# Performance work log

Hardware: AMD Instinct MI355X
Metric: run time of the kernel (lower is better)

## Reference

```python
import jax, jax.numpy as jnp
import numpy as np

N = 4096
IN_F = 256
F = 64      # out_features
H = 4       # heads
NEG_SLOPE = 0.2


def setup_inputs() -> dict:
    key = jax.random.key(0)
    k1, k2, k3, k4 = jax.random.split(key, 4)
    x = jax.random.normal(k1, (N, IN_F), dtype=jnp.float32)
    # symmetric random binary adjacency with self-loops (avoids empty softmax rows)
    adj = jax.random.bernoulli(k2, 0.5, (N, N)).astype(jnp.float32)
    adj = jnp.clip(adj + adj.T, 0.0, 1.0)
    adj = jnp.maximum(adj, jnp.eye(N, dtype=jnp.float32))
    W = jax.random.normal(k3, (IN_F, F * H), dtype=jnp.float32) * (1.0 / np.sqrt(IN_F))
    a = jax.random.normal(k4, (2 * F, 1), dtype=jnp.float32) * 0.1
    return {"x": x, "adj": adj, "W": W, "a": a}


def reference(x, adj, W, a):
    # h: [N, H, F]
    h = (x @ W).reshape(N, H, F)
    # e[i, j, h] = leakyrelu(a_l . h[i, h] + a_r . h[j, h])  -- avoids the O(N^2*H*2F) concat
    a_l = a[:F, 0]
    a_r = a[F:, 0]
    el = jnp.einsum('nhf,f->nh', h, a_l)  # [N, H]
    er = jnp.einsum('nhf,f->nh', h, a_r)  # [N, H]
    e = jax.nn.leaky_relu(el[:, None, :] + er[None, :, :], NEG_SLOPE)  # [N, N, H]
    e = jnp.where(adj[:, :, None] == 0, -jnp.inf, e)
    attention = jax.nn.softmax(e, axis=1)  # softmax over neighbors j
    h_prime = jnp.einsum('ijh,jhf->ihf', attention, h)  # [N, H, F]
    return h_prime.mean(axis=1)  # [N, F]  (heads > 1 -> mean over heads)
```

## Files before the change

kernel.cpp:

```cpp
#include <hip/hip_runtime.h>
#include <hip/hip_bf16.h>

#define NN 4096
#define LOG2E 1.44269504088896340736f
#define SPLITS 16

typedef __attribute__((ext_vector_type(8))) short s8v;
typedef __attribute__((ext_vector_type(4))) float f4v;

__device__ __forceinline__ unsigned fu(float x){ union{float f;unsigned u;}z; z.f=x; return z.u; }
__device__ __forceinline__ unsigned short f2bf_rne(float x){
  unsigned u = fu(x);
  u += 0x7fffu + ((u >> 16) & 1u);
  return (unsigned short)(u >> 16);
}
__device__ __forceinline__ unsigned pack2_rne(float a, float b){
  return (unsigned)f2bf_rne(a) | ((unsigned)f2bf_rne(b) << 16);
}

__global__ __launch_bounds__(256) void k1_proj(
    const float* __restrict__ x, const float* __restrict__ W,
    const float* __restrict__ a, unsigned short* __restrict__ Vf,
    float* __restrict__ el4, float* __restrict__ Qr, float* __restrict__ Sr)
{
  __shared__ float4 xs[512];
  const int t = threadIdx.x;
  const int r0 = blockIdx.x * 8;
  const float4* xg = (const float4*)(x + (size_t)r0 * 256);
  xs[t] = xg[t];
  xs[t + 256] = xg[t + 256];
  __syncthreads();

  float acc[8] = {0.f,0.f,0.f,0.f,0.f,0.f,0.f,0.f};
  const float* Wp = W + t;
  float w0 = Wp[0], w1 = Wp[256], w2 = Wp[512], w3 = Wp[768];
  #pragma unroll 1
  for (int k4 = 0; k4 < 64; ++k4) {
    const int kn = (k4 + 1) & 63;
    float nw0 = Wp[kn*1024 +   0];
    float nw1 = Wp[kn*1024 + 256];
    float nw2 = Wp[kn*1024 + 512];
    float nw3 = Wp[kn*1024 + 768];
    #pragma unroll
    for (int r = 0; r < 8; ++r) {
      float4 xv = xs[r*64 + k4];
      acc[r] = fmaf(xv.x, w0, acc[r]);
      acc[r] = fmaf(xv.y, w1, acc[r]);
      acc[r] = fmaf(xv.z, w2, acc[r]);
      acc[r] = fmaf(xv.w, w3, acc[r]);
    }
    w0 = nw0; w1 = nw1; w2 = nw2; w3 = nw3;
  }

  union { unsigned u[4]; s8v v; } pk;
  #pragma unroll
  for (int p = 0; p < 4; ++p)
    pk.u[p] = pack2_rne(acc[2*p], acc[2*p+1]);
  {
    const int hh = t >> 6, nf = (t >> 4) & 3, mm = t & 15;
    const int jblk = r0 >> 5, qq = (r0 >> 3) & 3;
    const size_t chunk = (size_t)(((hh * 128 + jblk) * 4 + nf) * 64 + qq * 16 + mm);
    *(s8v*)(Vf + chunk * 8) = pk.v;
  }

  const int f = t & 63, h = t >> 6;
  const float al = a[f], ar = a[64 + f];
  #pragma unroll
  for (int r = 0; r < 8; ++r) {
    float v = acc[r] * al;
    float u = acc[r] * ar;
    #pragma unroll
    for (int off = 32; off > 0; off >>= 1) {
      v += __shfl_xor(v, off);
      u += __shfl_xor(u, off);
    }
    if (f == 0) {
      el4[(r0 + r) * 4 + h] = v * LOG2E;
      float up = u * LOG2E;
      Qr[h * NN + (r0 + r)] = __builtin_amdgcn_exp2f(up);
      Sr[h * NN + (r0 + r)] = __builtin_amdgcn_exp2f(0.2f * up);
    }
  }
}

__global__ __launch_bounds__(256, 4) void k0_pack(
    const float* __restrict__ adj, const float* __restrict__ el4,
    const float* __restrict__ Qr, const float* __restrict__ Sr,
    unsigned long long* __restrict__ adjB,
    float* __restrict__ PL, float* __restrict__ RL)
{
  const int t = threadIdx.x;
  const int w = t >> 6, l = t & 63;
  const int row = blockIdx.x * 4 + w;
  const float* arow = adj + (size_t)row * NN;

  float4 elv = *(const float4*)(el4 + row * 4);
  const float P[4] = { __builtin_amdgcn_exp2f(elv.x), __builtin_amdgcn_exp2f(elv.y),
                       __builtin_amdgcn_exp2f(elv.z), __builtin_amdgcn_exp2f(elv.w) };
  const float R[4] = { __builtin_amdgcn_exp2f(0.2f*elv.x), __builtin_amdgcn_exp2f(0.2f*elv.y),
                       __builtin_amdgcn_exp2f(0.2f*elv.z), __builtin_amdgcn_exp2f(0.2f*elv.w) };
  float lsum[4] = {0.f, 0.f, 0.f, 0.f};

  float4 av, qv0, qv1, qv2, qv3, sv0, sv1, sv2, sv3;
  av  = *(const float4*)(arow + l * 4);
  qv0 = *(const float4*)(Qr + 0 * NN + l * 4);
  qv1 = *(const float4*)(Qr + 1 * NN + l * 4);
  qv2 = *(const float4*)(Qr + 2 * NN + l * 4);
  qv3 = *(const float4*)(Qr + 3 * NN + l * 4);
  sv0 = *(const float4*)(Sr + 0 * NN + l * 4);
  sv1 = *(const float4*)(Sr + 1 * NN + l * 4);
  sv2 = *(const float4*)(Sr + 2 * NN + l * 4);
  sv3 = *(const float4*)(Sr + 3 * NN + l * 4);

  #pragma unroll 1
  for (int p = 0; p < 16; ++p) {
    const int nb = ((p < 15) ? (p + 1) * 256 : 0) + l * 4;
    float4 nav  = *(const float4*)(arow + nb);
    float4 nqv0 = *(const float4*)(Qr + 0 * NN + nb);
    float4 nqv1 = *(const float4*)(Qr + 1 * NN + nb);
    float4 nqv2 = *(const float4*)(Qr + 2 * NN + nb);
    float4 nqv3 = *(const float4*)(Qr + 3 * NN + nb);
    float4 nsv0 = *(const float4*)(Sr + 0 * NN + nb);
    float4 nsv1 = *(const float4*)(Sr + 1 * NN + nb);
    float4 nsv2 = *(const float4*)(Sr + 2 * NN + nb);
    float4 nsv3 = *(const float4*)(Sr + 3 * NN + nb);

    unsigned long long b0 = __ballot(av.x != 0.0f);
    unsigned long long b1 = __ballot(av.y != 0.0f);
    unsigned long long b2 = __ballot(av.z != 0.0f);
    unsigned long long b3 = __ballot(av.w != 0.0f);
    if (l == 0) {
      unsigned long long* dst = adjB + (size_t)row * 64 + p * 4;
      dst[0] = b0; dst[1] = b1; dst[2] = b2; dst[3] = b3;
    }
    #pragma unroll
    for (int h = 0; h < 4; ++h) {
      const float4 qv = (h==0)?qv0:(h==1)?qv1:(h==2)?qv2:qv3;
      const float4 sv = (h==0)?sv0:(h==1)?sv1:(h==2)?sv2:sv3;
      float m0 = fmaxf(P[h] * qv.x, R[h] * sv.x);
      float m1 = fmaxf(P[h] * qv.y, R[h] * sv.y);
      float m2 = fmaxf(P[h] * qv.z, R[h] * sv.z);
      float m3 = fmaxf(P[h] * qv.w, R[h] * sv.w);
      lsum[h] = fmaf(av.x, m0, lsum[h]);
      lsum[h] = fmaf(av.y, m1, lsum[h]);
      lsum[h] = fmaf(av.z, m2, lsum[h]);
      lsum[h] = fmaf(av.w, m3, lsum[h]);
    }
    av = nav;
    qv0 = nqv0; qv1 = nqv1; qv2 = nqv2; qv3 = nqv3;
    sv0 = nsv0; sv1 = nsv1; sv2 = nsv2; sv3 = nsv3;
  }

  #pragma unroll
  for (int h = 0; h < 4; ++h) {
    float v = lsum[h];
    #pragma unroll
    for (int off = 32; off > 0; off >>= 1) v += __shfl_xor(v, off);
    lsum[h] = v;
  }
  if (l < 4) {
    float li = 1.0f / lsum[l];
    PL[row * 4 + l] = P[l] * li;
    RL[row * 4 + l] = R[l] * li;
  }
}

__global__ __launch_bounds__(256, 4) void k2_attn(
    const unsigned long long* __restrict__ adjB, const unsigned short* __restrict__ Vf,
    const float* __restrict__ PL, const float* __restrict__ RL,
    const float* __restrict__ Qr, const float* __restrict__ Sr,
    float* __restrict__ out)
{
  __shared__ float qs[2048];
  const int t = threadIdx.x;
  const int w = t >> 6, l = t & 63;
  const int m = l & 15, q = l >> 4;
  const int i0 = blockIdx.x * 64;
  const int split = blockIdx.y;
  const int i = i0 + w * 16 + m;
  const int jwin = split * 256;

  {
    const int h = t >> 6;
    float4 qv = *(const float4*)(Qr + h * NN + jwin + l * 4);
    float4 sv = *(const float4*)(Sr + h * NN + jwin + l * 4);
    const int jc = l >> 3, qq = (l >> 1) & 3, hp = (l & 1) * 4;
    float* cell = qs + ((h * 8 + jc) * 4 + qq) * 16;
    *(float4*)(cell + hp) = qv;
    *(float4*)(cell + 8 + hp) = sv;
  }

  float4 pl4 = *(const float4*)(PL + i * 4);
  float4 rl4 = *(const float4*)(RL + i * 4);
  const float Pl[4] = {pl4.x, pl4.y, pl4.z, pl4.w};
  const float Rl[4] = {rl4.x, rl4.y, rl4.z, rl4.w};

  const unsigned long long* bp = adjB + (size_t)i * 64 + split * 4;
  unsigned long long b0 = bp[0], b1 = bp[1], b2 = bp[2], b3 = bp[3];

  f4v acc[4];
  #pragma unroll
  for (int nf = 0; nf < 4; ++nf) acc[nf] = (f4v){0.f, 0.f, 0.f, 0.f};

  const s8v* vfp = (const s8v*)Vf;
  s8v Bc[4];
  #pragma unroll
  for (int nf = 0; nf < 4; ++nf)
    Bc[nf] = vfp[(size_t)((0 * 128 + split * 8 + 0) * 4 + nf) * 64 + l];

  __syncthreads();

  #pragma unroll 1
  for (int jc = 0; jc < 8; ++jc) {
    const unsigned sh = jc * 8 + q * 2;
    const unsigned t0 = (unsigned)(b0 >> sh) & 3u;
    const unsigned t1 = (unsigned)(b1 >> sh) & 3u;
    const unsigned t2 = (unsigned)(b2 >> sh) & 3u;
    const unsigned t3 = (unsigned)(b3 >> sh) & 3u;
    float bitf[8];
    bitf[0] = (float)(t0 & 1u); bitf[4] = (float)(t0 >> 1);
    bitf[1] = (float)(t1 & 1u); bitf[5] = (float)(t1 >> 1);
    bitf[2] = (float)(t2 & 1u); bitf[6] = (float)(t2 >> 1);
    bitf[3] = (float)(t3 & 1u); bitf[7] = (float)(t3 >> 1);

    #pragma unroll
    for (int h = 0; h < 4; ++h) {
      const int hn = (h < 3) ? h + 1 : 0;
      const int jcn = (h < 3) ? jc : jc + 1;
      s8v Bn[4];
      #pragma unroll
      for (int nf = 0; nf < 4; ++nf)
        Bn[nf] = vfp[(size_t)((hn * 128 + split * 8 + jcn) * 4 + nf) * 64 + l];

      const float* cell = qs + ((h * 8 + jc) * 4 + q) * 16;
      float4 q0  = *(const float4*)(cell);
      float4 q1  = *(const float4*)(cell + 4);
      float4 sv0 = *(const float4*)(cell + 8);
      float4 sv1 = *(const float4*)(cell + 12);
      const float Ph = Pl[h], Rh = Rl[h];
      float s0 = bitf[0] * fmaxf(Ph * q0.x, Rh * sv0.x);
      float s1 = bitf[1] * fmaxf(Ph * q0.y, Rh * sv0.y);
      float s2 = bitf[2] * fmaxf(Ph * q0.z, Rh * sv0.z);
      float s3 = bitf[3] * fmaxf(Ph * q0.w, Rh * sv0.w);
      float s4 = bitf[4] * fmaxf(Ph * q1.x, Rh * sv1.x);
      float s5 = bitf[5] * fmaxf(Ph * q1.y, Rh * sv1.y);
      float s6 = bitf[6] * fmaxf(Ph * q1.z, Rh * sv1.z);
      float s7 = bitf[7] * fmaxf(Ph * q1.w, Rh * sv1.w);
      union { unsigned u[4]; s8v v; } A;
      A.u[0] = pack2_rne(s0, s1);
      A.u[1] = pack2_rne(s2, s3);
      A.u[2] = pack2_rne(s4, s5);
      A.u[3] = pack2_rne(s6, s7);
      #pragma unroll
      for (int nf = 0; nf < 4; ++nf)
        acc[nf] = __builtin_amdgcn_mfma_f32_16x16x32_bf16(A.v, Bc[nf], acc[nf], 0, 0, 0);
      #pragma unroll
      for (int nf = 0; nf < 4; ++nf) Bc[nf] = Bn[nf];
    }
  }

  #pragma unroll
  for (int nf = 0; nf < 4; ++nf)
    #pragma unroll
    for (int r = 0; r < 4; ++r) {
      int row = i0 + w * 16 + q * 4 + r;
      int col = nf * 16 + m;
      atomicAdd(&out[row * 64 + col], 0.25f * acc[nf][r]);
    }
}

extern "C" void kernel_launch(void* const* d_in, const int* in_sizes, int n_in,
                              void* d_out, int out_size, void* d_ws, size_t ws_size,
                              hipStream_t stream) {
  const float* x   = (const float*)d_in[0];
  const float* adj = (const float*)d_in[1];
  const float* W   = (const float*)d_in[2];
  const float* a   = (const float*)d_in[3];
  float* out = (float*)d_out;

  char* ws = (char*)d_ws;
  unsigned short* Vf = (unsigned short*)ws;
  float* el4 = (float*)(ws + (2u << 20));
  float* Qr  = (float*)(ws + (2u << 20) + (64u << 10));
  float* Sr  = (float*)(ws + (2u << 20) + (128u << 10));
  float* PLp = (float*)(ws + (2u << 20) + (192u << 10));
  float* RLp = (float*)(ws + (2u << 20) + (256u << 10));
  unsigned long long* adjB = (unsigned long long*)(ws + (2u << 20) + (320u << 10));

  hipMemsetAsync(out, 0, (size_t)out_size * sizeof(float), stream);
  k1_proj<<<512, 256, 0, stream>>>(x, W, a, Vf, el4, Qr, Sr);
  k0_pack<<<1024, 256, 0, stream>>>(adj, el4, Qr, Sr, adjB, PLp, RLp);
  k2_attn<<<dim3(64, SPLITS), 256, 0, stream>>>(adjB, Vf, PLp, RLp, Qr, Sr, out);
}
```

Before: 175.4 us.

## Remap attention waves to split the neighbor axis and reduce partials in LDS

In the attention kernel, the four waves of a block now take 16 rows each over four different 256-column neighbor windows, where before they took four row groups over one shared window. Each wave stages its own Q/S window in a larger shared buffer, which removes the early barrier. Partial accumulators are summed across waves in LDS before one wave issues the atomics, so global atomic traffic drops by a factor of four. The cost is four times the LDS footprint, which may lower occupancy, and less reuse of the Vf tiles across waves in a block.

```diff
diff --git a/kernel.cpp b/kernel.cpp
--- a/kernel.cpp
+++ b/kernel.cpp
@@ -3,7 +3,6 @@
 
 #define NN 4096
 #define LOG2E 1.44269504088896340736f
-#define SPLITS 16
 
 typedef __attribute__((ext_vector_type(8))) short s8v;
 typedef __attribute__((ext_vector_type(4))) float f4v;
@@ -171,23 +170,25 @@
     const float* __restrict__ Qr, const float* __restrict__ Sr,
     float* __restrict__ out)
 {
-  __shared__ float qs[2048];
+  __shared__ float qs[8192];
   const int t = threadIdx.x;
   const int w = t >> 6, l = t & 63;
   const int m = l & 15, q = l >> 4;
-  const int i0 = blockIdx.x * 64;
-  const int split = blockIdx.y;
-  const int i = i0 + w * 16 + m;
-  const int jwin = split * 256;
+  const int i0 = blockIdx.x * 16;
+  const int sw = blockIdx.y * 4 + w;
+  const int i = i0 + m;
+  const int jwin = sw * 256;
 
   {
-    const int h = t >> 6;
-    float4 qv = *(const float4*)(Qr + h * NN + jwin + l * 4);
-    float4 sv = *(const float4*)(Sr + h * NN + jwin + l * 4);
     const int jc = l >> 3, qq = (l >> 1) & 3, hp = (l & 1) * 4;
-    float* cell = qs + ((h * 8 + jc) * 4 + qq) * 16;
-    *(float4*)(cell + hp) = qv;
-    *(float4*)(cell + 8 + hp) = sv;
+    #pragma unroll
+    for (int h = 0; h < 4; ++h) {
+      float4 qv = *(const float4*)(Qr + h * NN + jwin + l * 4);
+      float4 sv = *(const float4*)(Sr + h * NN + jwin + l * 4);
+      float* cell = qs + (((w * 4 + h) * 8 + jc) * 4 + qq) * 16;
+      *(float4*)(cell + hp) = qv;
+      *(float4*)(cell + 8 + hp) = sv;
+    }
   }
 
   float4 pl4 = *(const float4*)(PL + i * 4);
@@ -195,7 +196,7 @@
   const float Pl[4] = {pl4.x, pl4.y, pl4.z, pl4.w};
   const float Rl[4] = {rl4.x, rl4.y, rl4.z, rl4.w};
 
-  const unsigned long long* bp = adjB + (size_t)i * 64 + split * 4;
+  const unsigned long long* bp = adjB + (size_t)i * 64 + sw * 4;
   unsigned long long b0 = bp[0], b1 = bp[1], b2 = bp[2], b3 = bp[3];
 
   f4v acc[4];
@@ -206,9 +207,7 @@
   s8v Bc[4];
   #pragma unroll
   for (int nf = 0; nf < 4; ++nf)
-    Bc[nf] = vfp[(size_t)((0 * 128 + split * 8 + 0) * 4 + nf) * 64 + l];
-
-  __syncthreads();
+    Bc[nf] = vfp[(size_t)((0 * 128 + sw * 8 + 0) * 4 + nf) * 64 + l];
 
   #pragma unroll 1
   for (int jc = 0; jc < 8; ++jc) {
@@ -230,9 +229,9 @@
       s8v Bn[4];
       #pragma unroll
       for (int nf = 0; nf < 4; ++nf)
-        Bn[nf] = vfp[(size_t)((hn * 128 + split * 8 + jcn) * 4 + nf) * 64 + l];
-
-      const float* cell = qs + ((h * 8 + jc) * 4 + q) * 16;
+        Bn[nf] = vfp[(size_t)((hn * 128 + sw * 8 + jcn) * 4 + nf) * 64 + l];
+
+      const float* cell = qs + (((w * 4 + h) * 8 + jc) * 4 + q) * 16;
       float4 q0  = *(const float4*)(cell);
       float4 q1  = *(const float4*)(cell + 4);
       float4 sv0 = *(const float4*)(cell + 8);
@@ -259,14 +258,30 @@
     }
   }
 
-  #pragma unroll
-  for (int nf = 0; nf < 4; ++nf)
-    #pragma unroll
-    for (int r = 0; r < 4; ++r) {
-      int row = i0 + w * 16 + q * 4 + r;
-      int col = nf * 16 + m;
-      atomicAdd(&out[row * 64 + col], 0.25f * acc[nf][r]);
-    }
+  __syncthreads();
+  if (w > 0) {
+    float* dst = qs + ((w - 1) * 64 + l) * 20;
+    #pragma unroll
+    for (int nf = 0; nf < 4; ++nf)
+      *(f4v*)(dst + nf * 4) = acc[nf];
+  }
+  __syncthreads();
+  if (w == 0) {
+    const float* src = qs + l * 20;
+    #pragma unroll
+    for (int nf = 0; nf < 4; ++nf) {
+      f4v s = acc[nf];
+      s += *(const f4v*)(src +    0 + nf * 4);
+      s += *(const f4v*)(src + 1280 + nf * 4);
+      s += *(const f4v*)(src + 2560 + nf * 4);
+      #pragma unroll
+      for (int r = 0; r < 4; ++r) {
+        int row = i0 + q * 4 + r;
+        int col = nf * 16 + m;
+        atomicAdd(&out[row * 64 + col], 0.25f * s[r]);
+      }
+    }
+  }
 }
 
 extern "C" void kernel_launch(void* const* d_in, const int* in_sizes, int n_in,
@@ -290,5 +305,5 @@
   hipMemsetAsync(out, 0, (size_t)out_size * sizeof(float), stream);
   k1_proj<<<512, 256, 0, stream>>>(x, W, a, Vf, el4, Qr, Sr);
   k0_pack<<<1024, 256, 0, stream>>>(adj, el4, Qr, Sr, adjB, PLp, RLp);
-  k2_attn<<<dim3(64, SPLITS), 256, 0, stream>>>(adjB, Vf, PLp, RLp, Qr, Sr, out);
-}
+  k2_attn<<<dim3(256, 4), 256, 0, stream>>>(adjB, Vf, PLp, RLp, Qr, Sr, out);
+}
```

Result: no change. 174.3 us (-0.6%).
